# Kernel optimization log

Hardware: AMD Instinct MI355X
Metric: run time of the kernel (lower is better)

## Reference

```python
import jax, jax.numpy as jnp
import numpy as np

SPATIAL_SHAPES = [(160, 160), (80, 80), (40, 40)]
D_MODEL = 256
N_HEADS = 8
N_LEVELS = 3
N_POINTS = 4
B = 1
SEQ = sum(h * w for h, w in SPATIAL_SHAPES)  # 33600


def setup_inputs() -> dict:
    key = jax.random.key(0)
    ks = jax.random.split(key, 10)
    f = jax.random.normal
    return {
        "hidden_states": f(ks[0], (B, SEQ, D_MODEL), jnp.float32),
        "encoder_hidden_states": f(ks[1], (B, SEQ, D_MODEL), jnp.float32),
        "position_embeddings": f(ks[2], (B, SEQ, D_MODEL), jnp.float32),
        "reference_points": jax.random.uniform(ks[3], (B, SEQ, N_LEVELS, 2), jnp.float32),
        "Wv": f(ks[4], (D_MODEL, D_MODEL), jnp.float32) * 0.02,
        "bv": jnp.zeros((D_MODEL,), jnp.float32),
        "Ws": f(ks[5], (N_HEADS * N_LEVELS * N_POINTS * 2, D_MODEL), jnp.float32) * 0.02,
        "bs": f(ks[6], (N_HEADS * N_LEVELS * N_POINTS * 2,), jnp.float32) * 2.0,
        "Wa": f(ks[7], (N_HEADS * N_LEVELS * N_POINTS, D_MODEL), jnp.float32) * 0.02,
        "ba": jnp.zeros((N_HEADS * N_LEVELS * N_POINTS,), jnp.float32),
        "Wo": f(ks[8], (D_MODEL, D_MODEL), jnp.float32) * 0.02,
        "bo": jnp.zeros((D_MODEL,), jnp.float32),
    }


def grid_sample_bilinear(img, grid):
    """torch.nn.functional.grid_sample, mode='bilinear', padding_mode='zeros', align_corners=False.
    img: [N, C, Hi, Wi]; grid: [N, Hg, Wg, 2] with (x, y) in [-1, 1]. Returns [N, C, Hg, Wg]."""
    N, C, Hi, Wi = img.shape
    x = (grid[..., 0] + 1.0) * (Wi * 0.5) - 0.5  # unnormalized pixel coords
    y = (grid[..., 1] + 1.0) * (Hi * 0.5) - 0.5
    x0f = jnp.floor(x)
    y0f = jnp.floor(y)
    x0 = x0f.astype(jnp.int32)
    y0 = y0f.astype(jnp.int32)
    wx1 = x - x0f
    wy1 = y - y0f
    imgc = jnp.transpose(img, (0, 2, 3, 1))  # [N, Hi, Wi, C]
    n_idx = jnp.arange(N)[:, None, None]

    def tap(xi, yi, w):
        valid = (xi >= 0) & (xi < Wi) & (yi >= 0) & (yi < Hi)
        xc = jnp.clip(xi, 0, Wi - 1)
        yc = jnp.clip(yi, 0, Hi - 1)
        v = imgc[n_idx, yc, xc]  # [N, Hg, Wg, C]
        return v * (w * valid.astype(img.dtype))[..., None]

    out = (tap(x0, y0, (1.0 - wx1) * (1.0 - wy1))
           + tap(x0 + 1, y0, wx1 * (1.0 - wy1))
           + tap(x0, y0 + 1, (1.0 - wx1) * wy1)
           + tap(x0 + 1, y0 + 1, wx1 * wy1))
    return jnp.transpose(out, (0, 3, 1, 2))  # [N, C, Hg, Wg]


def reference(hidden_states, encoder_hidden_states, position_embeddings, reference_points,
              Wv, bv, Ws, bs, Wa, ba, Wo, bo):
    hd = D_MODEL // N_HEADS
    LP = N_LEVELS * N_POINTS
    Q = SEQ

    hs = hidden_states + position_embeddings  # [B, Q, D]
    value = (encoder_hidden_states @ Wv.T + bv).reshape(B, SEQ, N_HEADS, hd)
    offsets = (hs @ Ws.T + bs).reshape(B * Q, N_HEADS, LP, 2)
    attn = jax.nn.softmax((hs @ Wa.T + ba).reshape(B, Q, N_HEADS, LP), axis=-1)

    # offset normalizer: [w, h] per level, broadcast over points
    norm = jnp.array([[w, h] for (h, w) in SPATIAL_SHAPES], jnp.float32)  # [L, 2]
    norm = jnp.broadcast_to(norm[:, None, :], (N_LEVELS, N_POINTS, 2)).reshape(1, 1, LP, 2)
    rp = reference_points.reshape(-1, N_LEVELS, 1, 2)
    rp = jnp.broadcast_to(rp, (B * Q, N_LEVELS, N_POINTS, 2)).reshape(B * Q, 1, LP, 2)
    loc = rp + offsets / norm                # [BQ, H, LP, 2]
    grids = 2.0 * loc - 1.0

    attn_t = jnp.transpose(attn, (0, 2, 1, 3)).reshape(B * N_HEADS, 1, Q, LP)

    sampled = []
    start = 0
    for lvl, (h, w) in enumerate(SPATIAL_SHAPES):
        v = value[:, start:start + h * w].reshape(B, h * w, N_HEADS * hd)
        v = jnp.transpose(v, (0, 2, 1)).reshape(B * N_HEADS, hd, h, w)
        g = jnp.transpose(grids[:, :, lvl * N_POINTS:(lvl + 1) * N_POINTS], (1, 0, 2, 3))  # [H, BQ, P, 2] (B=1)
        sampled.append(grid_sample_bilinear(v, g))  # [B*H, hd, Q, P]
        start += h * w

    out = (jnp.concatenate(sampled, axis=-1) * attn_t).sum(-1)  # [B*H, hd, Q]
    out = jnp.transpose(out.reshape(B, N_HEADS * hd, Q), (0, 2, 1))  # [B, Q, D]
    output = out @ Wo.T + bo
    return output, attn
```

## Files before the change

### kernel.cpp

```cpp
#include <hip/hip_runtime.h>
#include <math.h>

#define QSEQ 33600
#define NHEADS 8

typedef __attribute__((ext_vector_type(8))) short short8;
typedef __attribute__((ext_vector_type(4))) float floatx4;
typedef unsigned short ushort_t;

static __device__ __forceinline__ ushort_t f2bf(float f) {
  unsigned u = __float_as_uint(f);
  return (ushort_t)((u + 0x7FFF + ((u >> 16) & 1)) >> 16);
}

static __device__ __forceinline__ void gload_lds16(const void* g, void* l) {
  __builtin_amdgcn_global_load_lds((__attribute__((address_space(1))) void*)g,
                                   (__attribute__((address_space(3))) void*)l, 16, 0, 0);
}

template <int ASRC, int MODE>
__global__ __launch_bounds__(256) void gemm96(
    const void* __restrict__ A1, const float* __restrict__ A2,
    const ushort_t* __restrict__ Wb, const float* __restrict__ b1,
    const float* __restrict__ b2, void* __restrict__ C1,
    float* __restrict__ C2, int N) {
  extern __shared__ ushort_t smem[];
  ushort_t* As = smem;
  ushort_t* Bs = smem + 6144;

  const int tid = threadIdx.x;
  const int m0 = blockIdx.y * 96;
  const int n0 = blockIdx.x * 128;
  const int wv = tid >> 6, lane = tid & 63;
  const int wm = wv >> 1, wn = wv & 1;
  const int l16 = lane & 15, quad = lane >> 4;
  const int l8 = l16 & 7;

  const ushort_t* gAb[3];
  ushort_t* lAb[3];
  const float* gAf[3];
  const float* gAf2[3];
  ushort_t* lAf[3];
#pragma unroll
  for (int i = 0; i < 3; ++i) {
    const int c = tid + i * 256;
    const int row = c >> 3, s = c & 7;
    if (ASRC == 0) {
      const int gch = s ^ (row & 7);
      gAb[i] = (const ushort_t*)A1 + (size_t)(m0 + row) * 256 + gch * 8;
      lAb[i] = As + (wv * 64 + i * 256) * 8;
    } else {
      gAf[i] = (const float*)A1 + (size_t)(m0 + row) * 256 + s * 8;
      if (ASRC == 2) gAf2[i] = A2 + (size_t)(m0 + row) * 256 + s * 8;
      lAf[i] = As + row * 64 + (s ^ (row & 7)) * 8;
    }
  }
  const ushort_t* gB[4];
  ushort_t* lB[4];
#pragma unroll
  for (int j = 0; j < 4; ++j) {
    const int cb = wv * 256 + j * 64 + lane;
    const int br = cb >> 3;
    const int gch = (cb & 7) ^ (br & 7);
    gB[j] = Wb + (size_t)(n0 + br) * 256 + gch * 8;
    lB[j] = Bs + (wv * 256 + j * 64) * 8;
  }

  floatx4 acc[3][4];
#pragma unroll
  for (int i = 0; i < 3; ++i)
#pragma unroll
    for (int j = 0; j < 4; ++j) acc[i][j] = (floatx4)(0.f);

  for (int k0 = 0; k0 < 256; k0 += 64) {
    if (ASRC == 0) {
#pragma unroll
      for (int i = 0; i < 3; ++i) gload_lds16(gAb[i] + k0, lAb[i]);
    } else {
#pragma unroll
      for (int i = 0; i < 3; ++i) {
        const float4 x0 = *(const float4*)(gAf[i] + k0);
        const float4 x1 = *(const float4*)(gAf[i] + k0 + 4);
        float v[8] = {x0.x, x0.y, x0.z, x0.w, x1.x, x1.y, x1.z, x1.w};
        if (ASRC == 2) {
          const float4 y0 = *(const float4*)(gAf2[i] + k0);
          const float4 y1 = *(const float4*)(gAf2[i] + k0 + 4);
          v[0] += y0.x; v[1] += y0.y; v[2] += y0.z; v[3] += y0.w;
          v[4] += y1.x; v[5] += y1.y; v[6] += y1.z; v[7] += y1.w;
        }
        ushort_t t[8];
#pragma unroll
        for (int e = 0; e < 8; ++e) t[e] = f2bf(v[e]);
        *(short8*)lAf[i] = *(const short8*)t;
      }
    }
#pragma unroll
    for (int j = 0; j < 4; ++j) gload_lds16(gB[j] + k0, lB[j]);
    __syncthreads();

#pragma unroll
    for (int k32 = 0; k32 < 2; ++k32) {
      const int cx = ((k32 * 4 + quad) ^ l8) * 8;
      short8 a[3], b[4];
#pragma unroll
      for (int mi = 0; mi < 3; ++mi)
        a[mi] = *(const short8*)&As[(wm * 48 + mi * 16 + l16) * 64 + cx];
#pragma unroll
      for (int ni = 0; ni < 4; ++ni)
        b[ni] = *(const short8*)&Bs[(wn * 64 + ni * 16 + l16) * 64 + cx];
#pragma unroll
      for (int mi = 0; mi < 3; ++mi)
#pragma unroll
        for (int ni = 0; ni < 4; ++ni)
          acc[mi][ni] = __builtin_amdgcn_mfma_f32_16x16x32_bf16(a[mi], b[ni], acc[mi][ni], 0, 0, 0);
    }
    __syncthreads();
  }

  if (MODE == 0) {
    float* C = (float*)C1;
#pragma unroll
    for (int ni = 0; ni < 4; ++ni) {
      const int col = n0 + wn * 64 + ni * 16 + l16;
      const float bia = b1[col];
#pragma unroll
      for (int mi = 0; mi < 3; ++mi) {
        const int rr = m0 + wm * 48 + mi * 16 + quad * 4;
#pragma unroll
        for (int r = 0; r < 4; ++r)
          C[(size_t)(rr + r) * N + col] = acc[mi][ni][r] + bia;
      }
    }
  } else if (MODE == 1) {
    ushort_t* C = (ushort_t*)C1;
#pragma unroll
    for (int ni = 0; ni < 4; ++ni) {
      const int col = n0 + wn * 64 + ni * 16 + l16;
      const float bia = b1[col];
      const int h = col >> 5, ch = col & 31;
#pragma unroll
      for (int mi = 0; mi < 3; ++mi) {
        const int rr = m0 + wm * 48 + mi * 16 + quad * 4;
#pragma unroll
        for (int r = 0; r < 4; ++r)
          C[((size_t)h * QSEQ + rr + r) * 32 + ch] = f2bf(acc[mi][ni][r] + bia);
      }
    }
  } else {
    float* smf = (float*)smem;
#pragma unroll
    for (int ni = 0; ni < 4; ++ni) {
      const int col = n0 + wn * 64 + ni * 16 + l16;
      if (col < 96) {
        const float bia = b1[col];
#pragma unroll
        for (int mi = 0; mi < 3; ++mi) {
          const int lr = wm * 48 + mi * 16 + quad * 4;
#pragma unroll
          for (int r = 0; r < 4; ++r)
            smf[(lr + r) * 96 + col] = acc[mi][ni][r] + bia;
        }
      } else if (col < 288) {
        const float bia = b2[col - 96];
#pragma unroll
        for (int mi = 0; mi < 3; ++mi) {
          const int rr = m0 + wm * 48 + mi * 16 + quad * 4;
#pragma unroll
          for (int r = 0; r < 4; ++r)
            C2[(size_t)(rr + r) * 192 + (col - 96)] = acc[mi][ni][r] + bia;
        }
      }
    }
    __syncthreads();
    if (blockIdx.x == 0) {
      float* C = (float*)C1;
#pragma unroll
      for (int p = 0; p < 3; ++p) {
        const int task = tid + p * 256;
        const int row = task >> 3, hh = task & 7;
        float v[12];
        float mx = -1e30f;
#pragma unroll
        for (int i = 0; i < 12; ++i) {
          v[i] = smf[row * 96 + hh * 12 + i];
          mx = fmaxf(mx, v[i]);
        }
        float s = 0.f;
#pragma unroll
        for (int i = 0; i < 12; ++i) {
          v[i] = __expf(v[i] - mx);
          s += v[i];
        }
        const float inv = 1.f / s;
        float4 o[3];
#pragma unroll
        for (int i = 0; i < 3; ++i) {
          o[i].x = v[i * 4 + 0] * inv;
          o[i].y = v[i * 4 + 1] * inv;
          o[i].z = v[i * 4 + 2] * inv;
          o[i].w = v[i * 4 + 3] * inv;
        }
        float4* dst = (float4*)&C[(size_t)(m0 + row) * 96 + hh * 12];
        dst[0] = o[0];
        dst[1] = o[1];
        dst[2] = o[2];
      }
    }
  }
}

__global__ __launch_bounds__(256) void cvt_weights_kernel(
    const float* __restrict__ Wv, const float* __restrict__ Ws,
    const float* __restrict__ Wa, const float* __restrict__ Wo,
    ushort_t* __restrict__ o) {
  const int t = blockIdx.x * 256 + threadIdx.x;
  const int e = t * 4;
  if (e >= 204800) return;
  const float* src;
  int off;
  if (e < 65536)       { src = Wv; off = e; }
  else if (e < 90112)  { src = Wa; off = e - 65536; }
  else if (e < 139264) { src = Ws; off = e - 90112; }
  else                 { src = Wo; off = e - 139264; }
  const float4 x = *(const float4*)(src + off);
  ushort_t tmp[4] = {f2bf(x.x), f2bf(x.y), f2bf(x.z), f2bf(x.w)};
  *(uint2*)(o + e) = *(const uint2*)tmp;
}

__global__ __launch_bounds__(256) void msda_sample_kernel(
    const ushort_t* __restrict__ value,
    const float* __restrict__ sp,
    const float* __restrict__ attn,
    const float* __restrict__ refp,
    ushort_t* __restrict__ outp) {
  const int h = blockIdx.x & 7;
  const int q = (blockIdx.x >> 3) * 4 + (threadIdx.x >> 6);
  const int lane = threadIdx.x & 63;
  const int cg = lane >> 4, pt = lane & 15;
  const int ptc = pt < 12 ? pt : 11;
  const int lvl = ptc >> 2;
  const int S = lvl == 0 ? 160 : (lvl == 1 ? 80 : 40);
  const int base = lvl == 0 ? 0 : (lvl == 1 ? 25600 : 32000);

  float a = attn[q * 96 + h * 12 + ptc];
  a = pt < 12 ? a : 0.f;
  const float2 off = *(const float2*)&sp[q * 192 + h * 24 + ptc * 2];
  const float2 rp = *(const float2*)&refp[q * 6 + lvl * 2];

  const float x = fmaf(rp.x, (float)S, off.x) - 0.5f;
  const float y = fmaf(rp.y, (float)S, off.y) - 0.5f;
  const float xf = floorf(x), yf = floorf(y);
  const int x0 = (int)xf, y0 = (int)yf;
  const float wx1 = x - xf, wy1 = y - yf;

  const float wx0z = (x0 >= 0 && x0 < S) ? 1.f - wx1 : 0.f;
  const float wx1z = (x0 + 1 >= 0 && x0 + 1 < S) ? wx1 : 0.f;
  const float wy0z = (y0 >= 0 && y0 < S) ? 1.f - wy1 : 0.f;
  const float wy1z = (y0 + 1 >= 0 && y0 + 1 < S) ? wy1 : 0.f;

  const int x0c = min(max(x0, 0), S - 1);
  const int x1c = min(max(x0 + 1, 0), S - 1);
  const int y0c = min(max(y0, 0), S - 1);
  const int y1c = min(max(y0 + 1, 0), S - 1);

  const float w00 = a * wx0z * wy0z, w10 = a * wx1z * wy0z;
  const float w01 = a * wx0z * wy1z, w11 = a * wx1z * wy1z;

  const ushort_t* hb = value + ((h * QSEQ + base) << 5) + cg * 8;
  const int r0 = y0c * S, r1 = y1c * S;
  const uint4 u00 = *(const uint4*)(hb + ((r0 + x0c) << 5));
  const uint4 u10 = *(const uint4*)(hb + ((r0 + x1c) << 5));
  const uint4 u01 = *(const uint4*)(hb + ((r1 + x0c) << 5));
  const uint4 u11 = *(const uint4*)(hb + ((r1 + x1c) << 5));

  float facc[8];
  {
    const unsigned a0[4] = {u00.x, u00.y, u00.z, u00.w};
    const unsigned a1[4] = {u10.x, u10.y, u10.z, u10.w};
    const unsigned a2[4] = {u01.x, u01.y, u01.z, u01.w};
    const unsigned a3[4] = {u11.x, u11.y, u11.z, u11.w};
#pragma unroll
    for (int i = 0; i < 4; ++i) {
      float lo = __uint_as_float(a0[i] << 16) * w00;
      float hi = __uint_as_float(a0[i] & 0xFFFF0000u) * w00;
      lo = fmaf(__uint_as_float(a1[i] << 16), w10, lo);
      hi = fmaf(__uint_as_float(a1[i] & 0xFFFF0000u), w10, hi);
      lo = fmaf(__uint_as_float(a2[i] << 16), w01, lo);
      hi = fmaf(__uint_as_float(a2[i] & 0xFFFF0000u), w01, hi);
      lo = fmaf(__uint_as_float(a3[i] << 16), w11, lo);
      hi = fmaf(__uint_as_float(a3[i] & 0xFFFF0000u), w11, hi);
      facc[2 * i + 0] = lo;
      facc[2 * i + 1] = hi;
    }
  }

#pragma unroll
  for (int m = 1; m < 16; m <<= 1)
#pragma unroll
    for (int i = 0; i < 8; ++i) facc[i] += __shfl_xor(facc[i], m, 64);

  if (pt == 0) {
    ushort_t t[8];
#pragma unroll
    for (int i = 0; i < 8; ++i) t[i] = f2bf(facc[i]);
    *(uint4*)&outp[(size_t)q * 256 + h * 32 + cg * 8] = *(const uint4*)t;
  }
}

extern "C" void kernel_launch(void* const* d_in, const int* in_sizes, int n_in,
                              void* d_out, int out_size, void* d_ws, size_t ws_size,
                              hipStream_t stream) {
  const float* hidden = (const float*)d_in[0];
  const float* ehs    = (const float*)d_in[1];
  const float* pos    = (const float*)d_in[2];
  const float* refp   = (const float*)d_in[3];
  const float* Wv = (const float*)d_in[4];
  const float* bv = (const float*)d_in[5];
  const float* Ws = (const float*)d_in[6];
  const float* bs = (const float*)d_in[7];
  const float* Wa = (const float*)d_in[8];
  const float* ba = (const float*)d_in[9];
  const float* Wo = (const float*)d_in[10];
  const float* bo = (const float*)d_in[11];

  float* out  = (float*)d_out;
  float* attn = out + (size_t)QSEQ * 256;

  char* ws = (char*)d_ws;
  ushort_t* ws_value = (ushort_t*)ws;
  ushort_t* ws_outp  = ws_value + (size_t)QSEQ * 256;
  ushort_t* ws_w     = ws_outp + (size_t)QSEQ * 256;
  float* ws_sp = (float*)(ws_w + 204800);

  ushort_t* Wv_b = ws_w;
  ushort_t* Wm_b = ws_w + 65536;
  ushort_t* Wo_b = ws_w + 139264;

  dim3 blk(256);

  cvt_weights_kernel<<<dim3(200), blk, 0, stream>>>(Wv, Ws, Wa, Wo, ws_w);

  gemm96<1, 1><<<dim3(2, 350), blk, 28672, stream>>>(ehs, nullptr, Wv_b, bv, nullptr, ws_value, nullptr, 256);
  gemm96<2, 2><<<dim3(3, 350), blk, 36864, stream>>>(hidden, pos, Wm_b, ba, bs, attn, ws_sp, 288);
  msda_sample_kernel<<<dim3((QSEQ / 4) * 8), blk, 0, stream>>>(ws_value, ws_sp, attn, refp, ws_outp);
  gemm96<0, 0><<<dim3(2, 350), blk, 28672, stream>>>(ws_outp, nullptr, Wo_b, bo, nullptr, out, nullptr, 256);
}
```

Measured before the change: 312.0 us.

## Fuse value and sampling-offset GEMMs, convert weights to bf16 inside GEMM tiles

Removes the separate weight-conversion kernel and instead loads fp32 weights in each GEMM block, converting them to bf16 on the fly before the LDS store. The value projection and the attention/offset projection are merged into one launch, with the grid's x-index choosing which GEMM each block runs. This cuts two launches and the serialization between them. In exchange, every block redundantly reads fp32 weights (twice the bytes) and converts them, and the B tile loses the async global-to-LDS path.

```diff
diff --git a/kernel.cpp b/kernel.cpp
--- a/kernel.cpp
+++ b/kernel.cpp
@@ -2,7 +2,6 @@
 #include <math.h>
 
 #define QSEQ 33600
-#define NHEADS 8
 
 typedef __attribute__((ext_vector_type(8))) short short8;
 typedef __attribute__((ext_vector_type(4))) float floatx4;
@@ -19,51 +18,62 @@
 }
 
 template <int ASRC, int MODE>
-__global__ __launch_bounds__(256) void gemm96(
-    const void* __restrict__ A1, const float* __restrict__ A2,
-    const ushort_t* __restrict__ Wb, const float* __restrict__ b1,
-    const float* __restrict__ b2, void* __restrict__ C1,
-    float* __restrict__ C2, int N) {
-  extern __shared__ ushort_t smem[];
+static __device__ __forceinline__ void gemm_body(
+    const int bx, const int by,
+    const float* __restrict__ A1, const float* __restrict__ A2,
+    const ushort_t* __restrict__ Ab,
+    const float* __restrict__ B1, const float* __restrict__ B2, const int bsplit,
+    const float* __restrict__ b1, const float* __restrict__ b2,
+    void* __restrict__ C1, float* __restrict__ C2, const int N,
+    ushort_t* smem) {
   ushort_t* As = smem;
   ushort_t* Bs = smem + 6144;
 
   const int tid = threadIdx.x;
-  const int m0 = blockIdx.y * 96;
-  const int n0 = blockIdx.x * 128;
+  const int m0 = by * 96;
+  const int n0 = bx * 128;
   const int wv = tid >> 6, lane = tid & 63;
   const int wm = wv >> 1, wn = wv & 1;
   const int l16 = lane & 15, quad = lane >> 4;
   const int l8 = l16 & 7;
 
-  const ushort_t* gAb[3];
-  ushort_t* lAb[3];
   const float* gAf[3];
   const float* gAf2[3];
-  ushort_t* lAf[3];
+  const ushort_t* gAb[3];
+  ushort_t* lA[3];
 #pragma unroll
   for (int i = 0; i < 3; ++i) {
     const int c = tid + i * 256;
     const int row = c >> 3, s = c & 7;
     if (ASRC == 0) {
-      const int gch = s ^ (row & 7);
-      gAb[i] = (const ushort_t*)A1 + (size_t)(m0 + row) * 256 + gch * 8;
-      lAb[i] = As + (wv * 64 + i * 256) * 8;
+      gAb[i] = Ab + (size_t)(m0 + row) * 256 + ((s ^ (row & 7)) * 8);
+      lA[i] = As + (wv * 64 + i * 256) * 8;
     } else {
-      gAf[i] = (const float*)A1 + (size_t)(m0 + row) * 256 + s * 8;
+      gAf[i] = A1 + (size_t)(m0 + row) * 256 + s * 8;
       if (ASRC == 2) gAf2[i] = A2 + (size_t)(m0 + row) * 256 + s * 8;
-      lAf[i] = As + row * 64 + (s ^ (row & 7)) * 8;
-    }
-  }
-  const ushort_t* gB[4];
-  ushort_t* lB[4];
+      lA[i] = As + row * 64 + (s ^ (row & 7)) * 8;
+    }
+  }
+  const float* gBf[4];
+  ushort_t* lBf[4];
 #pragma unroll
   for (int j = 0; j < 4; ++j) {
-    const int cb = wv * 256 + j * 64 + lane;
-    const int br = cb >> 3;
-    const int gch = (cb & 7) ^ (br & 7);
-    gB[j] = Wb + (size_t)(n0 + br) * 256 + gch * 8;
-    lB[j] = Bs + (wv * 256 + j * 64) * 8;
+    const int c = tid + j * 256;
+    const int row = c >> 3, s = c & 7;
+    const int grow = n0 + row;
+    const float* bsrc;
+    int r2;
+    if (grow < bsplit) {
+      bsrc = B1;
+      r2 = grow;
+    } else {
+      bsrc = B2;
+      r2 = grow - bsplit;
+      const int rmax = N - bsplit - 1;
+      if (r2 > rmax) r2 = rmax;
+    }
+    gBf[j] = bsrc + (size_t)r2 * 256 + s * 8;
+    lBf[j] = Bs + row * 64 + (s ^ (row & 7)) * 8;
   }
 
   floatx4 acc[3][4];
@@ -75,7 +85,7 @@
   for (int k0 = 0; k0 < 256; k0 += 64) {
     if (ASRC == 0) {
 #pragma unroll
-      for (int i = 0; i < 3; ++i) gload_lds16(gAb[i] + k0, lAb[i]);
+      for (int i = 0; i < 3; ++i) gload_lds16(gAb[i] + k0, lA[i]);
     } else {
 #pragma unroll
       for (int i = 0; i < 3; ++i) {
@@ -91,11 +101,17 @@
         ushort_t t[8];
 #pragma unroll
         for (int e = 0; e < 8; ++e) t[e] = f2bf(v[e]);
-        *(short8*)lAf[i] = *(const short8*)t;
-      }
-    }
-#pragma unroll
-    for (int j = 0; j < 4; ++j) gload_lds16(gB[j] + k0, lB[j]);
+        *(short8*)lA[i] = *(const short8*)t;
+      }
+    }
+#pragma unroll
+    for (int j = 0; j < 4; ++j) {
+      const float4 x0 = *(const float4*)(gBf[j] + k0);
+      const float4 x1 = *(const float4*)(gBf[j] + k0 + 4);
+      ushort_t t[8] = {f2bf(x0.x), f2bf(x0.y), f2bf(x0.z), f2bf(x0.w),
+                       f2bf(x1.x), f2bf(x1.y), f2bf(x1.z), f2bf(x1.w)};
+      *(short8*)lBf[j] = *(const short8*)t;
+    }
     __syncthreads();
 
 #pragma unroll
@@ -172,7 +188,7 @@
       }
     }
     __syncthreads();
-    if (blockIdx.x == 0) {
+    if (bx == 0) {
       float* C = (float*)C1;
 #pragma unroll
       for (int p = 0; p < 3; ++p) {
@@ -209,22 +225,29 @@
   }
 }
 
-__global__ __launch_bounds__(256) void cvt_weights_kernel(
-    const float* __restrict__ Wv, const float* __restrict__ Ws,
-    const float* __restrict__ Wa, const float* __restrict__ Wo,
-    ushort_t* __restrict__ o) {
-  const int t = blockIdx.x * 256 + threadIdx.x;
-  const int e = t * 4;
-  if (e >= 204800) return;
-  const float* src;
-  int off;
-  if (e < 65536)       { src = Wv; off = e; }
-  else if (e < 90112)  { src = Wa; off = e - 65536; }
-  else if (e < 139264) { src = Ws; off = e - 90112; }
-  else                 { src = Wo; off = e - 139264; }
-  const float4 x = *(const float4*)(src + off);
-  ushort_t tmp[4] = {f2bf(x.x), f2bf(x.y), f2bf(x.z), f2bf(x.w)};
-  *(uint2*)(o + e) = *(const uint2*)tmp;
+__global__ __launch_bounds__(256) void pre_gemms(
+    const float* __restrict__ ehs, const float* __restrict__ hidden,
+    const float* __restrict__ pos,
+    const float* __restrict__ Wv, const float* __restrict__ bv,
+    const float* __restrict__ Wa, const float* __restrict__ ba,
+    const float* __restrict__ Ws, const float* __restrict__ bs,
+    ushort_t* __restrict__ value, float* __restrict__ attn,
+    float* __restrict__ sp) {
+  extern __shared__ ushort_t smem[];
+  if (blockIdx.x < 2)
+    gemm_body<1, 1>(blockIdx.x, blockIdx.y, ehs, nullptr, nullptr,
+                    Wv, Wv, 1 << 30, bv, nullptr, value, nullptr, 256, smem);
+  else
+    gemm_body<2, 2>(blockIdx.x - 2, blockIdx.y, hidden, pos, nullptr,
+                    Wa, Ws, 96, ba, bs, attn, sp, 288, smem);
+}
+
+__global__ __launch_bounds__(256) void out_gemm(
+    const ushort_t* __restrict__ samp, const float* __restrict__ Wo,
+    const float* __restrict__ bo, float* __restrict__ out) {
+  extern __shared__ ushort_t smem[];
+  gemm_body<0, 0>(blockIdx.x, blockIdx.y, nullptr, nullptr, samp,
+                  Wo, Wo, 1 << 30, bo, nullptr, out, nullptr, 256, smem);
 }
 
 __global__ __launch_bounds__(256) void msda_sample_kernel(
@@ -329,19 +352,13 @@
   char* ws = (char*)d_ws;
   ushort_t* ws_value = (ushort_t*)ws;
   ushort_t* ws_outp  = ws_value + (size_t)QSEQ * 256;
-  ushort_t* ws_w     = ws_outp + (size_t)QSEQ * 256;
-  float* ws_sp = (float*)(ws_w + 204800);
-
-  ushort_t* Wv_b = ws_w;
-  ushort_t* Wm_b = ws_w + 65536;
-  ushort_t* Wo_b = ws_w + 139264;
+  float* ws_sp = (float*)(ws_outp + (size_t)QSEQ * 256);
 
   dim3 blk(256);
 
-  cvt_weights_kernel<<<dim3(200), blk, 0, stream>>>(Wv, Ws, Wa, Wo, ws_w);
-
-  gemm96<1, 1><<<dim3(2, 350), blk, 28672, stream>>>(ehs, nullptr, Wv_b, bv, nullptr, ws_value, nullptr, 256);
-  gemm96<2, 2><<<dim3(3, 350), blk, 36864, stream>>>(hidden, pos, Wm_b, ba, bs, attn, ws_sp, 288);
-  msda_sample_kernel<<<dim3((QSEQ / 4) * 8), blk, 0, stream>>>(ws_value, ws_sp, attn, refp, ws_outp);
-  gemm96<0, 0><<<dim3(2, 350), blk, 28672, stream>>>(ws_outp, nullptr, Wo_b, bo, nullptr, out, nullptr, 256);
-}
+  pre_gemms<<<dim3(5, 350), blk, 36864, stream>>>(
+      ehs, hidden, pos, Wv, bv, Wa, ba, Ws, bs, ws_value, attn, ws_sp);
+  msda_sample_kernel<<<dim3((QSEQ / 4) * 8), blk, 0, stream>>>(
+      ws_value, ws_sp, attn, refp, ws_outp);
+  out_gemm<<<dim3(2, 350), blk, 28672, stream>>>(ws_outp, Wo, bo, out);
+}
```

Result: faster. 299.5 us (-4.0%).
